# Optimization experiments

Measured on AMD Instinct MI355X. Metric: run time of the kernel, lower is better.

Reference implementation:

```python
import jax, jax.numpy as jnp
import numpy as np

EPS = 1e-4
B, C, H, W = 8, 192, 64, 64
HID, DE, N_CLS, CLS_F, E = 256, 64, 8192, 128, 131072
N_IMG = B * H * W


def geolin(x, w):
    # MP_GeoLinear forward: weight-normalized linear, recomputed each call.
    fan = w.shape[1]
    n = jnp.linalg.norm(w, axis=1, keepdims=True)           # per-output-row norm (fp32)
    wn = w / (EPS + n / np.sqrt(fan))                       # normalize() with alpha=1/sqrt(fan)
    return x @ (wn * (1.0 / np.sqrt(fan))).T                # gain/sqrt(fan_in)


def mp_silu(x):
    return jax.nn.silu(x) / 0.596


def mp_cat(a, b, t=0.5):
    Na, Nb = a.shape[1], b.shape[1]
    Cc = np.sqrt((Na + Nb) / ((1 - t) ** 2 + t ** 2))
    return jnp.concatenate([(Cc / np.sqrt(Na) * (1 - t)) * a,
                            (Cc / np.sqrt(Nb) * t) * b], axis=1)


def hetero_conv(x_src, x_dst, src, dst, ea, wl, wr, n_dst):
    # MP_HIPGnnConv: gather -> mp_cat with edge_attr -> mean aggregate -> lin_l,
    # mp_sum with lin_r(x_dst) -> L2 normalize (normalize=True).
    msg = mp_cat(x_src[src], ea)                            # [E, HID+DE]
    s = jax.ops.segment_sum(msg, dst, num_segments=n_dst)
    cnt = jax.ops.segment_sum(jnp.ones((msg.shape[0],), msg.dtype), dst, num_segments=n_dst)
    agg = s / jnp.maximum(cnt, 1.0)[:, None]                # scatter-mean (empty rows -> 0)
    out = (geolin(agg, wl) + geolin(x_dst, wr)) / np.sqrt(2.0)  # mp_sum(t=0.5)
    return out / jnp.maximum(jnp.linalg.norm(out, axis=-1, keepdims=True), 1e-12)


def forward(x, class_x, ea_c2i, ea_i2c,
            w_in_img, w_in_cls,
            wl_c2i_1, wr_c2i_1, wl_i2c_1, wr_i2c_1,
            wl_c2i_2, wr_c2i_2, wl_i2c_2, wr_i2c_2,
            w_out_img, w_out_cls,
            src_c2i, dst_c2i, src_i2c, dst_i2c):
    b, c, h, w = x.shape
    n_img = b * h * w
    n_cls = class_x.shape[0]
    # image pixels become 'image_node' features: [B,C,H,W] -> [B*H*W, C]
    h_img = geolin(jnp.transpose(x, (0, 2, 3, 1)).reshape(-1, c), w_in_img)
    h_cls = geolin(class_x, w_in_cls)
    layers = [(wl_c2i_1, wr_c2i_1, wl_i2c_1, wr_i2c_1),
              (wl_c2i_2, wr_c2i_2, wl_i2c_2, wr_i2c_2)]
    for wl_ci, wr_ci, wl_ic, wr_ic in layers:
        a_img, a_cls = mp_silu(h_img), mp_silu(h_cls)
        h_img = hetero_conv(a_cls, a_img, src_c2i, dst_c2i, ea_c2i, wl_ci, wr_ci, n_img)
        h_cls = hetero_conv(a_img, a_cls, src_i2c, dst_i2c, ea_i2c, wl_ic, wr_ic, n_cls)
    out_img = geolin(h_img, w_out_img).reshape(b, h, w, -1)
    out_img = jnp.transpose(out_img, (0, 3, 1, 2))          # extract_image_nodes
    out_cls = geolin(h_cls, w_out_cls)
    return out_img, out_cls


def setup_inputs() -> dict:
    key = jax.random.key(0)
    ks = jax.random.split(key, 24)
    d = {
        'x': jax.random.normal(ks[0], (B, C, H, W), jnp.float32),
        'class_x': jax.random.normal(ks[1], (N_CLS, CLS_F), jnp.float32),
        'ea_c2i': jax.random.normal(ks[2], (E, DE), jnp.float32),
        'ea_i2c': jax.random.normal(ks[3], (E, DE), jnp.float32),
        'w_in_img': jax.random.normal(ks[4], (HID, C), jnp.float32),
        'w_in_cls': jax.random.normal(ks[5], (HID, CLS_F), jnp.float32),
        'wl_c2i_1': jax.random.normal(ks[6], (HID, HID + DE), jnp.float32),
        'wr_c2i_1': jax.random.normal(ks[7], (HID, HID), jnp.float32),
        'wl_i2c_1': jax.random.normal(ks[8], (HID, HID + DE), jnp.float32),
        'wr_i2c_1': jax.random.normal(ks[9], (HID, HID), jnp.float32),
        'wl_c2i_2': jax.random.normal(ks[10], (HID, HID + DE), jnp.float32),
        'wr_c2i_2': jax.random.normal(ks[11], (HID, HID), jnp.float32),
        'wl_i2c_2': jax.random.normal(ks[12], (HID, HID + DE), jnp.float32),
        'wr_i2c_2': jax.random.normal(ks[13], (HID, HID), jnp.float32),
        'w_out_img': jax.random.normal(ks[14], (HID, HID), jnp.float32),
        'w_out_cls': jax.random.normal(ks[15], (HID, HID), jnp.float32),
        'src_c2i': jax.random.randint(ks[16], (E,), 0, N_CLS, jnp.int32),
        'dst_c2i': jax.random.randint(ks[17], (E,), 0, N_IMG, jnp.int32),
        'src_i2c': jax.random.randint(ks[18], (E,), 0, N_IMG, jnp.int32),
        'dst_i2c': jax.random.randint(ks[19], (E,), 0, N_CLS, jnp.int32),
    }
    return d


def reference(x, class_x, ea_c2i, ea_i2c,
              w_in_img, w_in_cls,
              wl_c2i_1, wr_c2i_1, wl_i2c_1, wr_i2c_1,
              wl_c2i_2, wr_c2i_2, wl_i2c_2, wr_i2c_2,
              w_out_img, w_out_cls,
              src_c2i, dst_c2i, src_i2c, dst_i2c):
    return forward(x, class_x, ea_c2i, ea_i2c,
                   w_in_img, w_in_cls,
                   wl_c2i_1, wr_c2i_1, wl_i2c_1, wr_i2c_1,
                   wl_c2i_2, wr_c2i_2, wl_i2c_2, wr_i2c_2,
                   w_out_img, w_out_cls,
                   src_c2i, dst_c2i, src_i2c, dst_i2c)
```

## Files before the change

kernel.cpp:

```cpp
#include <hip/hip_runtime.h>
#include <cmath>

constexpr int CIN  = 192;
constexpr int HW   = 4096;
constexpr int NIMG = 32768;
constexpr int NCLS = 8192;
constexpr int NE   = 131072;

#define EPSW 1e-4f
#define ALPHA 0.7905694150420949f
#define BETA  1.5811388300841898f
#define SILU_INV 1.6778523489932886f

using bf16x8 = __attribute__((ext_vector_type(8))) __bf16;
using f32x4  = __attribute__((ext_vector_type(4))) float;

__device__ __forceinline__ ushort f2bf(float f) {
  uint u = __float_as_uint(f);
  u = (u + 0x7FFFu + ((u >> 16) & 1u)) >> 16;
  return (ushort)u;
}
__device__ __forceinline__ float bf2f(ushort h) {
  return __uint_as_float(((uint)h) << 16);
}
__device__ __forceinline__ float wave_red_sum(float v) {
  #pragma unroll
  for (int off = 32; off > 0; off >>= 1) v += __shfl_xor(v, off, 64);
  return v;
}
__device__ __forceinline__ int wave_red_sumi(int v) {
  #pragma unroll
  for (int off = 32; off > 0; off >>= 1) v += __shfl_xor(v, off, 64);
  return v;
}
__device__ __forceinline__ uint4 packbf8(float a0, float a1, float a2, float a3,
                                         float a4, float a5, float a6, float a7) {
  uint4 r;
  r.x = (uint)f2bf(a0) | ((uint)f2bf(a1) << 16);
  r.y = (uint)f2bf(a2) | ((uint)f2bf(a3) << 16);
  r.z = (uint)f2bf(a4) | ((uint)f2bf(a5) << 16);
  r.w = (uint)f2bf(a6) | ((uint)f2bf(a7) << 16);
  return r;
}

struct WNA {
  const float* w[12];
  ushort* o[12];
  int F[12];
  int os[12];
  int oo[12];
};
__global__ __launch_bounds__(256) void pre_k(WNA a,
                                             const int* __restrict__ d1,
                                             const int* __restrict__ d2,
                                             int* __restrict__ c1,
                                             int* __restrict__ c2) {
  const int bx = blockIdx.x, t = threadIdx.x;
  if (bx < 768) {
    const int wi = bx >> 6;
    const int row = ((bx & 63) << 2) + (t >> 6);
    const int lane = t & 63;
    const int F = a.F[wi];
    const float* wr = a.w[wi] + (size_t)row * F;
    float ss = 0.f;
    for (int f = lane; f < F; f += 64) { float v = wr[f]; ss += v * v; }
    ss = wave_red_sum(ss);
    const float scale = 1.0f / (EPSW * sqrtf((float)F) + sqrtf(ss));
    ushort* o = a.o[wi] + (size_t)row * a.os[wi] + a.oo[wi];
    for (int f = lane; f < F; f += 64) o[f] = f2bf(wr[f] * scale);
  } else {
    const int e = (bx - 768) * 256 + t;
    atomicAdd(&c1[d1[e]], 1);
    atomicAdd(&c2[d2[e]], 1);
  }
}

__global__ __launch_bounds__(256) void scanA_k(const int* __restrict__ cnt,
                                               int* __restrict__ st_img,
                                               int* __restrict__ st_cls,
                                               int* __restrict__ bsum) {
  const int bid = blockIdx.x;
  const bool cls = bid >= 32;
  const int* c = cnt + (cls ? NIMG : 0);
  int* s = cls ? st_cls : st_img;
  const int base = (cls ? bid - 32 : bid) * 1024;
  const int t = threadIdx.x, lane = t & 63, wid = t >> 6;
  int4 v = *(const int4*)(c + base + t * 4);
  const int i0 = v.x, i1 = i0 + v.y, i2 = i1 + v.z, i3 = i2 + v.w;
  int x = i3;
  #pragma unroll
  for (int off = 1; off < 64; off <<= 1) {
    int y = __shfl_up(x, off, 64);
    if (lane >= off) x += y;
  }
  const int pre = x - i3;
  __shared__ int wt[4];
  if (lane == 63) wt[wid] = x;
  __syncthreads();
  int woff = 0;
  #pragma unroll
  for (int i = 0; i < 4; ++i) if (i < wid) woff += wt[i];
  const int b = woff + pre;
  int4 o = { b, b + i0, b + i1, b + i2 };
  *(int4*)(s + base + t * 4) = o;
  if (t == 255) bsum[bid] = woff + x;
}

__global__ __launch_bounds__(256) void scanC_k(const int* __restrict__ bsum,
                                               int* __restrict__ st_img,
                                               int* __restrict__ st_cls) {
  const int bid = blockIdx.x;
  const bool cls = bid >= 32;
  const int seg0 = cls ? 32 : 0;
  const int t = threadIdx.x;
  __shared__ int off_s;
  if (t < 64) {
    int v = (t < bid - seg0) ? bsum[seg0 + t] : 0;
    v = wave_red_sumi(v);
    if (t == 0) off_s = v;
  }
  __syncthreads();
  const int off = off_s;
  int* s = cls ? st_cls : st_img;
  const int base = (cls ? bid - 32 : bid) * 1024;
  int4 v = *(int4*)(s + base + t * 4);
  v.x += off; v.y += off; v.z += off; v.w += off;
  *(int4*)(s + base + t * 4) = v;
  if (bid == 0 && t == 0) { st_img[NIMG] = NE; st_cls[NCLS] = NE; }
}

__global__ void fill2_k(const int* __restrict__ dst1, const int* __restrict__ src1,
                        const int* __restrict__ st1, int* __restrict__ cur1,
                        int2* __restrict__ eix1,
                        const int* __restrict__ dst2, const int* __restrict__ src2,
                        const int* __restrict__ st2, int* __restrict__ cur2,
                        int2* __restrict__ eix2) {
  int e = blockIdx.x * 256 + threadIdx.x;
  int d = dst1[e];
  int p = atomicAdd(&cur1[d], 1);
  eix1[st1[d] + p] = make_int2(e, src1[e]);
  d = dst2[e];
  p = atomicAdd(&cur2[d], 1);
  eix2[st2[d] + p] = make_int2(e, src2[e]);
}

__global__ __launch_bounds__(256) void agg2_k(
    const ushort* __restrict__ Aimg, const ushort* __restrict__ Acls,
    const int2* __restrict__ eix_ci, const int2* __restrict__ eix_ic,
    const int* __restrict__ st_img, const int* __restrict__ st_cls,
    ushort* __restrict__ agg_img, ushort* __restrict__ agg_cls,
    const float* __restrict__ ea_ci, const float* __restrict__ ea_ic,
    ushort* __restrict__ eam_img, ushort* __restrict__ eam_cls, int do_eam) {
  const int row  = blockIdx.x * 4 + (threadIdx.x >> 6);
  const int lane = threadIdx.x & 63;
  const ushort* Hs; const int2* eix; const int* st; ushort* out;
  const float* EA; ushort* oute; int r;
  if (row < NIMG) { r = row;        Hs = Acls; eix = eix_ci; st = st_img;
                    out = agg_img + (size_t)r * 256; EA = ea_ci;
                    oute = eam_img + (size_t)r * 64; }
  else            { r = row - NIMG; Hs = Aimg; eix = eix_ic; st = st_cls;
                    out = agg_cls + (size_t)r * 256; EA = ea_ic;
                    oute = eam_cls + (size_t)r * 64; }
  const int s0 = st[r], s1 = st[r + 1];
  float a0 = 0, a1 = 0, a2 = 0, a3 = 0, ae = 0;
  for (int j = s0; j < s1; j += 4) {
    const int i1 = min(j + 1, s1 - 1), i2 = min(j + 2, s1 - 1), i3 = min(j + 3, s1 - 1);
    const int2 e0 = eix[j], e1 = eix[i1], e2 = eix[i2], e3 = eix[i3];
    const float w1 = (j + 1 < s1) ? 1.f : 0.f;
    const float w2 = (j + 2 < s1) ? 1.f : 0.f;
    const float w3 = (j + 3 < s1) ? 1.f : 0.f;
    ushort4 h0 = *(const ushort4*)(Hs + (size_t)e0.y * 256 + lane * 4);
    ushort4 h1 = *(const ushort4*)(Hs + (size_t)e1.y * 256 + lane * 4);
    ushort4 h2 = *(const ushort4*)(Hs + (size_t)e2.y * 256 + lane * 4);
    ushort4 h3 = *(const ushort4*)(Hs + (size_t)e3.y * 256 + lane * 4);
    a0 += bf2f(h0.x) + w1 * bf2f(h1.x) + w2 * bf2f(h2.x) + w3 * bf2f(h3.x);
    a1 += bf2f(h0.y) + w1 * bf2f(h1.y) + w2 * bf2f(h2.y) + w3 * bf2f(h3.y);
    a2 += bf2f(h0.z) + w1 * bf2f(h1.z) + w2 * bf2f(h2.z) + w3 * bf2f(h3.z);
    a3 += bf2f(h0.w) + w1 * bf2f(h1.w) + w2 * bf2f(h2.w) + w3 * bf2f(h3.w);
    if (do_eam) {
      ae += EA[(size_t)e0.x * 64 + lane] + w1 * EA[(size_t)e1.x * 64 + lane]
          + w2 * EA[(size_t)e2.x * 64 + lane] + w3 * EA[(size_t)e3.x * 64 + lane];
    }
  }
  const float inv = 1.0f / fmaxf((float)(s1 - s0), 1.0f);
  const float c = ALPHA * inv;
  ushort4 o = { f2bf(a0 * c), f2bf(a1 * c), f2bf(a2 * c), f2bf(a3 * c) };
  *(ushort4*)(out + lane * 4) = o;
  if (do_eam) oute[lane] = f2bf(ae * BETA * inv);
}

__device__ __forceinline__ int lds_swz(int row, int kbyte) {
  return ((row << 6) + kbyte) ^ ((row & 7) << 4);
}

struct FJ {
  const ushort* AD; const ushort* AG; const ushort* EAM;
  const float* AF; const ushort* B; ushort* O;
  int K, a_mode, do_norm, do_silu;
};

__device__ __forceinline__ void fgemm_body(const FJ J, int bx, char* ldsb) {
  ushort* As = (ushort*)ldsb;
  ushort* Bs = (ushort*)(ldsb + 8192);
  const int t    = threadIdx.x;
  const int row0 = bx * 128;
  const int srowA = t >> 2, skA = (t & 3) * 8;
  const int srowB = t >> 1, skB = (t & 1) * 16;
  const int wid = t >> 6, lane = t & 63;
  const int wr = (wid >> 2) * 64, wcq = wid & 3, wc = wcq * 64;
  const int l15 = lane & 15, q = lane >> 4, lk16 = q * 16;
  const int K = J.K;
  f32x4 acc[4][4] = {};

  uint4 areg, breg0, breg1;
  auto loadA = [&](int k0) {
    const int row = row0 + srowA;
    if (J.a_mode == 2) {
      const int kk = k0 + skA;
      const ushort* p = (kk < 256) ? J.AG + (size_t)row * 256 + kk
                      : (kk < 320) ? J.EAM + (size_t)row * 64 + (kk - 256)
                                   : J.AD + (size_t)row * 256 + (kk - 320);
      areg = *(const uint4*)p;
    } else if (J.a_mode == 3) {
      const float* p = J.AF + (size_t)row * K + k0 + skA;
      float4 f0 = *(const float4*)p;
      float4 f1 = *(const float4*)(p + 4);
      areg = packbf8(f0.x, f0.y, f0.z, f0.w, f1.x, f1.y, f1.z, f1.w);
    } else {
      const int b = row >> 12, hw = row & 4095;
      const float* p = J.AF + ((size_t)(b * CIN + k0 + skA)) * HW + hw;
      float f0 = p[0], f1 = p[HW], f2 = p[2 * HW], f3 = p[3 * HW];
      float f4 = p[4 * HW], f5 = p[5 * HW], f6 = p[6 * HW], f7 = p[7 * HW];
      areg = packbf8(f0, f1, f2, f3, f4, f5, f6, f7);
    }
  };
  auto loadB = [&](int k0) {
    const ushort* p = J.B + (size_t)srowB * K + k0 + skB;
    breg0 = *(const uint4*)p;
    breg1 = *(const uint4*)(p + 8);
  };

  loadA(0); loadB(0);
  for (int k0 = 0; k0 < K; k0 += 32) {
    __syncthreads();
    *(uint4*)(ldsb + lds_swz(srowA, skA * 2)) = areg;
    *(uint4*)((char*)Bs + lds_swz(srowB, skB * 2)) = breg0;
    *(uint4*)((char*)Bs + lds_swz(srowB, skB * 2 + 16)) = breg1;
    __syncthreads();
    if (k0 + 32 < K) { loadA(k0 + 32); loadB(k0 + 32); }
    bf16x8 af[4], bfr[4];
    #pragma unroll
    for (int m = 0; m < 4; ++m)
      af[m] = *(const bf16x8*)((const char*)As + lds_swz(wr + m * 16 + l15, lk16));
    #pragma unroll
    for (int n = 0; n < 4; ++n)
      bfr[n] = *(const bf16x8*)((const char*)Bs + lds_swz(wc + n * 16 + l15, lk16));
    #pragma unroll
    for (int m = 0; m < 4; ++m)
      #pragma unroll
      for (int n = 0; n < 4; ++n)
        acc[m][n] = __builtin_amdgcn_mfma_f32_16x16x32_bf16(af[m], bfr[n], acc[m][n], 0, 0, 0);
  }

  float sc_row[4][4];
  #pragma unroll
  for (int m = 0; m < 4; ++m)
    #pragma unroll
    for (int j = 0; j < 4; ++j) sc_row[m][j] = 1.0f;
  if (J.do_norm) {
    __syncthreads();
    float* part = (float*)ldsb;
    #pragma unroll
    for (int m = 0; m < 4; ++m)
      #pragma unroll
      for (int j = 0; j < 4; ++j) {
        float ss = 0.f;
        #pragma unroll
        for (int n = 0; n < 4; ++n) { float v = acc[m][n][j]; ss += v * v; }
        ss += __shfl_xor(ss, 1, 64); ss += __shfl_xor(ss, 2, 64);
        ss += __shfl_xor(ss, 4, 64); ss += __shfl_xor(ss, 8, 64);
        if (l15 == 0) part[(wr + m * 16 + q * 4 + j) * 4 + wcq] = ss;
      }
    __syncthreads();
    #pragma unroll
    for (int m = 0; m < 4; ++m)
      #pragma unroll
      for (int j = 0; j < 4; ++j) {
        float4 p4 = *(float4*)&part[(wr + m * 16 + q * 4 + j) * 4];
        sc_row[m][j] = 1.0f / fmaxf(sqrtf(p4.x + p4.y + p4.z + p4.w), 1e-12f);
      }
  }
  #pragma unroll
  for (int m = 0; m < 4; ++m)
    #pragma unroll
    for (int j = 0; j < 4; ++j) {
      const int r = row0 + wr + m * 16 + q * 4 + j;
      #pragma unroll
      for (int n = 0; n < 4; ++n) {
        float v = acc[m][n][j] * sc_row[m][j];
        if (J.do_silu) v = (v / (1.0f + __expf(-v))) * SILU_INV;
        J.O[(size_t)r * 256 + wc + n * 16 + l15] = f2bf(v);
      }
    }
}

__global__ __launch_bounds__(512) void fgemm2_k(FJ j0, FJ j1, int n0) {
  __shared__ char ldsb[24576];
  const int bx = blockIdx.x;
  if (bx < n0) fgemm_body(j0, bx, ldsb);
  else         fgemm_body(j1, bx - n0, ldsb);
}

__device__ __forceinline__ void mgemm_body(
    const ushort* __restrict__ A, const ushort* __restrict__ B,
    float* __restrict__ C, int K, int ldc, int c_mode,
    int row0, int col0, char* ldsb) {
  ushort* As = (ushort*)ldsb;
  ushort* Bs = (ushort*)(ldsb + 8192);
  const int t    = threadIdx.x;
  const int srow = t >> 1;
  const int skh  = (t & 1) * 16;
  const int w    = t >> 6, lane = t & 63;
  const int wr   = (w >> 1) * 64, wc = (w & 1) * 64;
  const int l15  = lane & 15, lk16 = (lane >> 4) * 16;
  f32x4 acc[4][4] = {};

  uint4 ar0, ar1, br0, br1;
  auto loadA = [&](int k0) {
    const ushort* p = A + (size_t)(row0 + srow) * K + k0 + skh;
    ar0 = *(const uint4*)(p);
    ar1 = *(const uint4*)(p + 8);
  };
  auto loadB = [&](int k0) {
    const ushort* p = B + (size_t)(col0 + srow) * K + k0 + skh;
    br0 = *(const uint4*)(p);
    br1 = *(const uint4*)(p + 8);
  };

  loadA(0); loadB(0);
  for (int k0 = 0; k0 < K; k0 += 32) {
    __syncthreads();
    *(uint4*)((char*)As + lds_swz(srow, skh * 2))      = ar0;
    *(uint4*)((char*)As + lds_swz(srow, skh * 2 + 16)) = ar1;
    *(uint4*)((char*)Bs + lds_swz(srow, skh * 2))      = br0;
    *(uint4*)((char*)Bs + lds_swz(srow, skh * 2 + 16)) = br1;
    __syncthreads();
    if (k0 + 32 < K) { loadA(k0 + 32); loadB(k0 + 32); }
    bf16x8 af[4], bfr[4];
    #pragma unroll
    for (int m = 0; m < 4; ++m)
      af[m] = *(const bf16x8*)((const char*)As + lds_swz(wr + m * 16 + l15, lk16));
    #pragma unroll
    for (int n = 0; n < 4; ++n)
      bfr[n] = *(const bf16x8*)((const char*)Bs + lds_swz(wc + n * 16 + l15, lk16));
    #pragma unroll
    for (int m = 0; m < 4; ++m)
      #pragma unroll
      for (int n = 0; n < 4; ++n)
        acc[m][n] = __builtin_amdgcn_mfma_f32_16x16x32_bf16(af[m], bfr[n], acc[m][n], 0, 0, 0);
  }

  #pragma unroll
  for (int m = 0; m < 4; ++m) {
    const int rbase = row0 + wr + m * 16 + (lane >> 4) * 4;
    #pragma unroll
    for (int n = 0; n < 4; ++n) {
      const int col = col0 + wc + n * 16 + l15;
      #pragma unroll
      for (int j = 0; j < 4; ++j) {
        const int r = rbase + j;
        if (c_mode == 1)
          C[((size_t)(col >> 12) * 256 + r) * 4096 + (col & 4095)] = acc[m][n][j];
        else
          C[(size_t)r * ldc + col] = acc[m][n][j];
      }
    }
  }
}

__global__ __launch_bounds__(256) void outproj_k(
    const ushort* __restrict__ Wimg, const ushort* __restrict__ Himg,
    float* __restrict__ Oimg, const ushort* __restrict__ Hcls,
    const ushort* __restrict__ Wcls, float* __restrict__ Ocls) {
  __shared__ char ldsb[16384];
  const int bx = blockIdx.x;
  if (bx < 512)
    mgemm_body(Wimg, Himg, Oimg, 256, 0, 1, (bx & 1) * 128, (bx >> 1) * 128, ldsb);
  else {
    const int b2 = bx - 512;
    mgemm_body(Hcls, Wcls, Ocls, 256, 256, 2, (b2 >> 1) * 128, (b2 & 1) * 128, ldsb);
  }
}

extern "C" void kernel_launch(void* const* d_in, const int* in_sizes, int n_in,
                              void* d_out, int out_size, void* d_ws, size_t ws_size,
                              hipStream_t stream) {
  const float* x        = (const float*)d_in[0];
  const float* class_x  = (const float*)d_in[1];
  const float* ea_c2i   = (const float*)d_in[2];
  const float* ea_i2c   = (const float*)d_in[3];
  const int* src_c2i = (const int*)d_in[16];
  const int* dst_c2i = (const int*)d_in[17];
  const int* src_i2c = (const int*)d_in[18];
  const int* dst_i2c = (const int*)d_in[19];

  float* ws = (float*)d_ws;
  size_t off = 0;
  auto alloc = [&](size_t n) { float* p = ws + off; off += (n + 15) & ~(size_t)15; return p; };

  ushort* A_img   = (ushort*)alloc((size_t)NIMG * 128);
  ushort* A_cls   = (ushort*)alloc((size_t)NCLS * 128);
  ushort* H_img   = (ushort*)alloc((size_t)NIMG * 128);
  ushort* H_cls   = (ushort*)alloc((size_t)NCLS * 128);
  ushort* agg_img = (ushort*)alloc((size_t)NIMG * 128);
  ushort* agg_cls = (ushort*)alloc((size_t)NCLS * 128);
  ushort* eam_img = (ushort*)alloc((size_t)NIMG * 32);
  ushort* eam_cls = (ushort*)alloc((size_t)NCLS * 32);
  int* cnt       = (int*)alloc(2 * (NIMG + NCLS));
  int* cur       = cnt + (NIMG + NCLS);
  int* bsum      = (int*)alloc(48);
  int* st_img    = (int*)alloc(NIMG + 1 + NCLS + 1 + 14);
  int* st_cls    = st_img + NIMG + 1;
  int2* eix_c2i  = (int2*)alloc((size_t)NE * 2);
  int2* eix_i2c  = (int2*)alloc((size_t)NE * 2);
  ushort* wn_in_img  = (ushort*)alloc(256 * 96);
  ushort* wn_in_cls  = (ushort*)alloc(256 * 64);
  ushort* wcat0      = (ushort*)alloc(256 * 288);
  ushort* wcat1      = (ushort*)alloc(256 * 288);
  ushort* wcat2      = (ushort*)alloc(256 * 288);
  ushort* wcat3      = (ushort*)alloc(256 * 288);
  ushort* wn_out_img = (ushort*)alloc(256 * 128);
  ushort* wn_out_cls = (ushort*)alloc(256 * 128);

  const dim3 blk(256);

  hipMemsetAsync(cnt, 0, (size_t)2 * (NIMG + NCLS) * sizeof(int), stream);
  WNA wa;
  const float* wsrc[12] = { (const float*)d_in[4], (const float*)d_in[5],
                            (const float*)d_in[6], (const float*)d_in[7],
                            (const float*)d_in[8], (const float*)d_in[9],
                            (const float*)d_in[10], (const float*)d_in[11],
                            (const float*)d_in[12], (const float*)d_in[13],
                            (const float*)d_in[14], (const float*)d_in[15] };
  ushort* wdst[12] = { wn_in_img, wn_in_cls, wcat0, wcat0, wcat1, wcat1,
                       wcat2, wcat2, wcat3, wcat3, wn_out_img, wn_out_cls };
  const int wF[12]  = { 192, 128, 320, 256, 320, 256, 320, 256, 320, 256, 256, 256 };
  const int wOS[12] = { 192, 128, 576, 576, 576, 576, 576, 576, 576, 576, 256, 256 };
  const int wOO[12] = { 0, 0, 0, 320, 0, 320, 0, 320, 0, 320, 0, 0 };
  for (int i = 0; i < 12; ++i) {
    wa.w[i] = wsrc[i]; wa.o[i] = wdst[i]; wa.F[i] = wF[i]; wa.os[i] = wOS[i]; wa.oo[i] = wOO[i];
  }
  pre_k<<<768 + NE / 256, blk, 0, stream>>>(wa, dst_c2i, dst_i2c, cnt, cnt + NIMG);

  scanA_k<<<40, blk, 0, stream>>>(cnt, st_img, st_cls, bsum);
  scanC_k<<<40, blk, 0, stream>>>(bsum, st_img, st_cls);
  fill2_k<<<NE / 256, blk, 0, stream>>>(dst_c2i, src_c2i, st_img, cur, eix_c2i,
                                        dst_i2c, src_i2c, st_cls, cur + NIMG, eix_i2c);

  FJ jin0 = { nullptr, nullptr, nullptr, x,       wn_in_img, A_img, 192, 1, 0, 1 };
  FJ jin1 = { nullptr, nullptr, nullptr, class_x, wn_in_cls, A_cls, 128, 3, 0, 1 };
  fgemm2_k<<<NIMG / 128 + NCLS / 128, 512, 0, stream>>>(jin0, jin1, NIMG / 128);

  agg2_k<<<(NIMG + NCLS) / 4, blk, 0, stream>>>(A_img, A_cls, eix_c2i, eix_i2c,
                                                st_img, st_cls, agg_img, agg_cls,
                                                ea_c2i, ea_i2c, eam_img, eam_cls, 1);
  FJ jc10 = { A_img, agg_img, eam_img, nullptr, wcat0, A_img, 576, 2, 1, 1 };
  FJ jc11 = { A_cls, agg_cls, eam_cls, nullptr, wcat1, A_cls, 576, 2, 1, 1 };
  fgemm2_k<<<NIMG / 128 + NCLS / 128, 512, 0, stream>>>(jc10, jc11, NIMG / 128);

  agg2_k<<<(NIMG + NCLS) / 4, blk, 0, stream>>>(A_img, A_cls, eix_c2i, eix_i2c,
                                                st_img, st_cls, agg_img, agg_cls,
                                                nullptr, nullptr, nullptr, nullptr, 0);
  FJ jc20 = { A_img, agg_img, eam_img, nullptr, wcat2, H_img, 576, 2, 1, 0 };
  FJ jc21 = { A_cls, agg_cls, eam_cls, nullptr, wcat3, H_cls, 576, 2, 1, 0 };
  fgemm2_k<<<NIMG / 128 + NCLS / 128, 512, 0, stream>>>(jc20, jc21, NIMG / 128);

  float* out_img = (float*)d_out;
  float* out_cls = (float*)d_out + (size_t)NIMG * 256;
  outproj_k<<<640, blk, 0, stream>>>(wn_out_img, H_img, out_img,
                                     H_cls, wn_out_cls, out_cls);
}
```

Before: 227.0 us.

## Unify GEMMs into double-buffered 64x256 tile kernel with pre-converted bf16 inputs

Replaces the 128x256 fused GEMM (512 threads) and the separate output-projection GEMM with one 256-thread kernel. It uses 64x256 tiles and double-buffers the LDS tiles, so each k-step needs one barrier instead of two. The input image is transposed and converted to bf16 in the preprocessing kernel, and class_x is converted there too, so GEMM A-loads become contiguous vector loads instead of strided fp32 gathers. This adds extra global write and read traffic for the staged inputs. Each block now covers fewer rows, which changes B-tile reuse and occupancy.

```diff
diff --git a/kernel.cpp b/kernel.cpp
--- a/kernel.cpp
+++ b/kernel.cpp
@@ -32,15 +32,6 @@
   #pragma unroll
   for (int off = 32; off > 0; off >>= 1) v += __shfl_xor(v, off, 64);
   return v;
-}
-__device__ __forceinline__ uint4 packbf8(float a0, float a1, float a2, float a3,
-                                         float a4, float a5, float a6, float a7) {
-  uint4 r;
-  r.x = (uint)f2bf(a0) | ((uint)f2bf(a1) << 16);
-  r.y = (uint)f2bf(a2) | ((uint)f2bf(a3) << 16);
-  r.z = (uint)f2bf(a4) | ((uint)f2bf(a5) << 16);
-  r.w = (uint)f2bf(a6) | ((uint)f2bf(a7) << 16);
-  return r;
 }
 
 struct WNA {
@@ -54,7 +45,12 @@
                                              const int* __restrict__ d1,
                                              const int* __restrict__ d2,
                                              int* __restrict__ c1,
-                                             int* __restrict__ c2) {
+                                             int* __restrict__ c2,
+                                             const float* __restrict__ x,
+                                             ushort* __restrict__ Xin,
+                                             const float* __restrict__ clsx,
+                                             ushort* __restrict__ clsb) {
+  __shared__ ushort T[192 * 65];
   const int bx = blockIdx.x, t = threadIdx.x;
   if (bx < 768) {
     const int wi = bx >> 6;
@@ -68,10 +64,31 @@
     const float scale = 1.0f / (EPSW * sqrtf((float)F) + sqrtf(ss));
     ushort* o = a.o[wi] + (size_t)row * a.os[wi] + a.oo[wi];
     for (int f = lane; f < F; f += 64) o[f] = f2bf(wr[f] * scale);
-  } else {
+  } else if (bx < 1280) {
     const int e = (bx - 768) * 256 + t;
     atomicAdd(&c1[d1[e]], 1);
     atomicAdd(&c2[d2[e]], 1);
+  } else if (bx < 1792) {
+    const int b2 = bx - 1280;
+    const int b = b2 >> 6, hw0 = (b2 & 63) * 64;
+    const float* xb = x + (size_t)b * CIN * HW;
+    for (int idx = t; idx < CIN * 64; idx += 256) {
+      int c = idx >> 6, p = idx & 63;
+      T[c * 65 + p] = f2bf(xb[(size_t)c * HW + hw0 + p]);
+    }
+    __syncthreads();
+    ushort* ob = Xin + ((size_t)b * HW + hw0) * CIN;
+    for (int idx = t; idx < CIN * 64; idx += 256) {
+      int p = idx / CIN, c = idx - p * CIN;
+      ob[(size_t)p * CIN + c] = T[c * 65 + p];
+    }
+  } else {
+    const int b3 = bx - 1792;
+    for (int i4 = b3 * 256 + t; i4 < (NCLS * 128) / 4; i4 += 128 * 256) {
+      float4 v = *(const float4*)(clsx + (size_t)i4 * 4);
+      ushort4 o = { f2bf(v.x), f2bf(v.y), f2bf(v.z), f2bf(v.w) };
+      *(ushort4*)(clsb + (size_t)i4 * 4) = o;
+    }
   }
 }
 
@@ -193,73 +210,73 @@
   return ((row << 6) + kbyte) ^ ((row & 7) << 4);
 }
 
-struct FJ {
-  const ushort* AD; const ushort* AG; const ushort* EAM;
-  const float* AF; const ushort* B; ushort* O;
-  int K, a_mode, do_norm, do_silu;
+struct GJ {
+  const ushort* A; const ushort* AG; const ushort* EAM; const ushort* B;
+  void* O;
+  int K, a_mode, c_mode, do_norm, do_silu, nrt;
 };
 
-__device__ __forceinline__ void fgemm_body(const FJ J, int bx, char* ldsb) {
-  ushort* As = (ushort*)ldsb;
-  ushort* Bs = (ushort*)(ldsb + 8192);
-  const int t    = threadIdx.x;
-  const int row0 = bx * 128;
-  const int srowA = t >> 2, skA = (t & 3) * 8;
-  const int srowB = t >> 1, skB = (t & 1) * 16;
+__device__ __forceinline__ void gemm_body(const GJ J, int bx, char* ldsb) {
+  const int t = threadIdx.x;
+  const int row0 = (bx % J.nrt) * 64;
+  const int col0 = (bx / J.nrt) * 256;
+  const int srowA = t >> 2, skA16 = (t & 3) * 16;
   const int wid = t >> 6, lane = t & 63;
-  const int wr = (wid >> 2) * 64, wcq = wid & 3, wc = wcq * 64;
+  const int wc = wid * 64;
   const int l15 = lane & 15, q = lane >> 4, lk16 = q * 16;
   const int K = J.K;
   f32x4 acc[4][4] = {};
-
-  uint4 areg, breg0, breg1;
+  uint4 ar, br0, br1, br2, br3;
+
   auto loadA = [&](int k0) {
     const int row = row0 + srowA;
+    const int kk = k0 + (skA16 >> 1);
     if (J.a_mode == 2) {
-      const int kk = k0 + skA;
       const ushort* p = (kk < 256) ? J.AG + (size_t)row * 256 + kk
                       : (kk < 320) ? J.EAM + (size_t)row * 64 + (kk - 256)
-                                   : J.AD + (size_t)row * 256 + (kk - 320);
-      areg = *(const uint4*)p;
-    } else if (J.a_mode == 3) {
-      const float* p = J.AF + (size_t)row * K + k0 + skA;
-      float4 f0 = *(const float4*)p;
-      float4 f1 = *(const float4*)(p + 4);
-      areg = packbf8(f0.x, f0.y, f0.z, f0.w, f1.x, f1.y, f1.z, f1.w);
+                                   : J.A + (size_t)row * 256 + (kk - 320);
+      ar = *(const uint4*)p;
     } else {
-      const int b = row >> 12, hw = row & 4095;
-      const float* p = J.AF + ((size_t)(b * CIN + k0 + skA)) * HW + hw;
-      float f0 = p[0], f1 = p[HW], f2 = p[2 * HW], f3 = p[3 * HW];
-      float f4 = p[4 * HW], f5 = p[5 * HW], f6 = p[6 * HW], f7 = p[7 * HW];
-      areg = packbf8(f0, f1, f2, f3, f4, f5, f6, f7);
+      ar = *(const uint4*)(J.A + (size_t)row * K + kk);
     }
   };
   auto loadB = [&](int k0) {
-    const ushort* p = J.B + (size_t)srowB * K + k0 + skB;
-    breg0 = *(const uint4*)p;
-    breg1 = *(const uint4*)(p + 8);
+    const ushort* p = J.B + (size_t)(col0 + t) * K + k0;
+    br0 = *(const uint4*)p;       br1 = *(const uint4*)(p + 8);
+    br2 = *(const uint4*)(p + 16); br3 = *(const uint4*)(p + 24);
   };
+  auto stage = [&](int buf) {
+    *(uint4*)(ldsb + buf * 4096 + lds_swz(srowA, skA16)) = ar;
+    char* bs = ldsb + 8192 + buf * 16384;
+    *(uint4*)(bs + lds_swz(t, 0))  = br0;
+    *(uint4*)(bs + lds_swz(t, 16)) = br1;
+    *(uint4*)(bs + lds_swz(t, 32)) = br2;
+    *(uint4*)(bs + lds_swz(t, 48)) = br3;
+  };
 
   loadA(0); loadB(0);
+  stage(0);
+  int cur = 0;
   for (int k0 = 0; k0 < K; k0 += 32) {
     __syncthreads();
-    *(uint4*)(ldsb + lds_swz(srowA, skA * 2)) = areg;
-    *(uint4*)((char*)Bs + lds_swz(srowB, skB * 2)) = breg0;
-    *(uint4*)((char*)Bs + lds_swz(srowB, skB * 2 + 16)) = breg1;
-    __syncthreads();
-    if (k0 + 32 < K) { loadA(k0 + 32); loadB(k0 + 32); }
+    const bool more = (k0 + 32) < K;
+    if (more) { loadA(k0 + 32); loadB(k0 + 32); }
+    const char* as = ldsb + cur * 4096;
+    const char* bs = ldsb + 8192 + cur * 16384;
     bf16x8 af[4], bfr[4];
     #pragma unroll
     for (int m = 0; m < 4; ++m)
-      af[m] = *(const bf16x8*)((const char*)As + lds_swz(wr + m * 16 + l15, lk16));
+      af[m] = *(const bf16x8*)(as + lds_swz(m * 16 + l15, lk16));
     #pragma unroll
     for (int n = 0; n < 4; ++n)
-      bfr[n] = *(const bf16x8*)((const char*)Bs + lds_swz(wc + n * 16 + l15, lk16));
+      bfr[n] = *(const bf16x8*)(bs + lds_swz(wc + n * 16 + l15, lk16));
     #pragma unroll
     for (int m = 0; m < 4; ++m)
       #pragma unroll
       for (int n = 0; n < 4; ++n)
         acc[m][n] = __builtin_amdgcn_mfma_f32_16x16x32_bf16(af[m], bfr[n], acc[m][n], 0, 0, 0);
+    if (more) stage(cur ^ 1);
+    cur ^= 1;
   }
 
   float sc_row[4][4];
@@ -279,117 +296,45 @@
         for (int n = 0; n < 4; ++n) { float v = acc[m][n][j]; ss += v * v; }
         ss += __shfl_xor(ss, 1, 64); ss += __shfl_xor(ss, 2, 64);
         ss += __shfl_xor(ss, 4, 64); ss += __shfl_xor(ss, 8, 64);
-        if (l15 == 0) part[(wr + m * 16 + q * 4 + j) * 4 + wcq] = ss;
+        if (l15 == 0) part[(m * 16 + q * 4 + j) * 4 + wid] = ss;
       }
     __syncthreads();
     #pragma unroll
     for (int m = 0; m < 4; ++m)
       #pragma unroll
       for (int j = 0; j < 4; ++j) {
-        float4 p4 = *(float4*)&part[(wr + m * 16 + q * 4 + j) * 4];
+        float4 p4 = *(float4*)&part[(m * 16 + q * 4 + j) * 4];
         sc_row[m][j] = 1.0f / fmaxf(sqrtf(p4.x + p4.y + p4.z + p4.w), 1e-12f);
       }
   }
+  ushort* Ob = (ushort*)J.O;
+  float*  Of = (float*)J.O;
   #pragma unroll
   for (int m = 0; m < 4; ++m)
     #pragma unroll
     for (int j = 0; j < 4; ++j) {
-      const int r = row0 + wr + m * 16 + q * 4 + j;
+      const int r = row0 + m * 16 + q * 4 + j;
       #pragma unroll
       for (int n = 0; n < 4; ++n) {
+        const int col = col0 + wc + n * 16 + l15;
         float v = acc[m][n][j] * sc_row[m][j];
-        if (J.do_silu) v = (v / (1.0f + __expf(-v))) * SILU_INV;
-        J.O[(size_t)r * 256 + wc + n * 16 + l15] = f2bf(v);
+        if (J.c_mode == 0) {
+          if (J.do_silu) v = (v / (1.0f + __expf(-v))) * SILU_INV;
+          Ob[(size_t)r * 256 + col] = f2bf(v);
+        } else if (J.c_mode == 1) {
+          Of[((size_t)(col >> 12) * 256 + r) * 4096 + (col & 4095)] = v;
+        } else {
+          Of[(size_t)r * 256 + col] = v;
+        }
       }
     }
 }
 
-__global__ __launch_bounds__(512) void fgemm2_k(FJ j0, FJ j1, int n0) {
-  __shared__ char ldsb[24576];
+__global__ __launch_bounds__(256) void gemm2_k(GJ j0, GJ j1, int n0) {
+  __shared__ char ldsb[40960];
   const int bx = blockIdx.x;
-  if (bx < n0) fgemm_body(j0, bx, ldsb);
-  else         fgemm_body(j1, bx - n0, ldsb);
-}
-
-__device__ __forceinline__ void mgemm_body(
-    const ushort* __restrict__ A, const ushort* __restrict__ B,
-    float* __restrict__ C, int K, int ldc, int c_mode,
-    int row0, int col0, char* ldsb) {
-  ushort* As = (ushort*)ldsb;
-  ushort* Bs = (ushort*)(ldsb + 8192);
-  const int t    = threadIdx.x;
-  const int srow = t >> 1;
-  const int skh  = (t & 1) * 16;
-  const int w    = t >> 6, lane = t & 63;
-  const int wr   = (w >> 1) * 64, wc = (w & 1) * 64;
-  const int l15  = lane & 15, lk16 = (lane >> 4) * 16;
-  f32x4 acc[4][4] = {};
-
-  uint4 ar0, ar1, br0, br1;
-  auto loadA = [&](int k0) {
-    const ushort* p = A + (size_t)(row0 + srow) * K + k0 + skh;
-    ar0 = *(const uint4*)(p);
-    ar1 = *(const uint4*)(p + 8);
-  };
-  auto loadB = [&](int k0) {
-    const ushort* p = B + (size_t)(col0 + srow) * K + k0 + skh;
-    br0 = *(const uint4*)(p);
-    br1 = *(const uint4*)(p + 8);
-  };
-
-  loadA(0); loadB(0);
-  for (int k0 = 0; k0 < K; k0 += 32) {
-    __syncthreads();
-    *(uint4*)((char*)As + lds_swz(srow, skh * 2))      = ar0;
-    *(uint4*)((char*)As + lds_swz(srow, skh * 2 + 16)) = ar1;
-    *(uint4*)((char*)Bs + lds_swz(srow, skh * 2))      = br0;
-    *(uint4*)((char*)Bs + lds_swz(srow, skh * 2 + 16)) = br1;
-    __syncthreads();
-    if (k0 + 32 < K) { loadA(k0 + 32); loadB(k0 + 32); }
-    bf16x8 af[4], bfr[4];
-    #pragma unroll
-    for (int m = 0; m < 4; ++m)
-      af[m] = *(const bf16x8*)((const char*)As + lds_swz(wr + m * 16 + l15, lk16));
-    #pragma unroll
-    for (int n = 0; n < 4; ++n)
-      bfr[n] = *(const bf16x8*)((const char*)Bs + lds_swz(wc + n * 16 + l15, lk16));
-    #pragma unroll
-    for (int m = 0; m < 4; ++m)
-      #pragma unroll
-      for (int n = 0; n < 4; ++n)
-        acc[m][n] = __builtin_amdgcn_mfma_f32_16x16x32_bf16(af[m], bfr[n], acc[m][n], 0, 0, 0);
-  }
-
-  #pragma unroll
-  for (int m = 0; m < 4; ++m) {
-    const int rbase = row0 + wr + m * 16 + (lane >> 4) * 4;
-    #pragma unroll
-    for (int n = 0; n < 4; ++n) {
-      const int col = col0 + wc + n * 16 + l15;
-      #pragma unroll
-      for (int j = 0; j < 4; ++j) {
-        const int r = rbase + j;
-        if (c_mode == 1)
-          C[((size_t)(col >> 12) * 256 + r) * 4096 + (col & 4095)] = acc[m][n][j];
-        else
-          C[(size_t)r * ldc + col] = acc[m][n][j];
-      }
-    }
-  }
-}
-
-__global__ __launch_bounds__(256) void outproj_k(
-    const ushort* __restrict__ Wimg, const ushort* __restrict__ Himg,
-    float* __restrict__ Oimg, const ushort* __restrict__ Hcls,
-    const ushort* __restrict__ Wcls, float* __restrict__ Ocls) {
-  __shared__ char ldsb[16384];
-  const int bx = blockIdx.x;
-  if (bx < 512)
-    mgemm_body(Wimg, Himg, Oimg, 256, 0, 1, (bx & 1) * 128, (bx >> 1) * 128, ldsb);
-  else {
-    const int b2 = bx - 512;
-    mgemm_body(Hcls, Wcls, Ocls, 256, 256, 2, (b2 >> 1) * 128, (b2 & 1) * 128, ldsb);
-  }
+  if (bx < n0) gemm_body(j0, bx, ldsb);
+  else         gemm_body(j1, bx - n0, ldsb);
 }
 
 extern "C" void kernel_launch(void* const* d_in, const int* in_sizes, int n_in,
@@ -431,6 +376,8 @@
   ushort* wcat3      = (ushort*)alloc(256 * 288);
   ushort* wn_out_img = (ushort*)alloc(256 * 128);
   ushort* wn_out_cls = (ushort*)alloc(256 * 128);
+  ushort* Xin      = agg_img;
+  ushort* class_bf = agg_cls;
 
   const dim3 blk(256);
 
@@ -450,33 +397,35 @@
   for (int i = 0; i < 12; ++i) {
     wa.w[i] = wsrc[i]; wa.o[i] = wdst[i]; wa.F[i] = wF[i]; wa.os[i] = wOS[i]; wa.oo[i] = wOO[i];
   }
-  pre_k<<<768 + NE / 256, blk, 0, stream>>>(wa, dst_c2i, dst_i2c, cnt, cnt + NIMG);
+  pre_k<<<1920, blk, 0, stream>>>(wa, dst_c2i, dst_i2c, cnt, cnt + NIMG,
+                                  x, Xin, class_x, class_bf);
 
   scanA_k<<<40, blk, 0, stream>>>(cnt, st_img, st_cls, bsum);
   scanC_k<<<40, blk, 0, stream>>>(bsum, st_img, st_cls);
   fill2_k<<<NE / 256, blk, 0, stream>>>(dst_c2i, src_c2i, st_img, cur, eix_c2i,
                                         dst_i2c, src_i2c, st_cls, cur + NIMG, eix_i2c);
 
-  FJ jin0 = { nullptr, nullptr, nullptr, x,       wn_in_img, A_img, 192, 1, 0, 1 };
-  FJ jin1 = { nullptr, nullptr, nullptr, class_x, wn_in_cls, A_cls, 128, 3, 0, 1 };
-  fgemm2_k<<<NIMG / 128 + NCLS / 128, 512, 0, stream>>>(jin0, jin1, NIMG / 128);
+  GJ jin0 = { Xin,      nullptr, nullptr, wn_in_img, A_img, 192, 0, 0, 0, 1, 512 };
+  GJ jin1 = { class_bf, nullptr, nullptr, wn_in_cls, A_cls, 128, 0, 0, 0, 1, 128 };
+  gemm2_k<<<640, blk, 0, stream>>>(jin0, jin1, 512);
 
   agg2_k<<<(NIMG + NCLS) / 4, blk, 0, stream>>>(A_img, A_cls, eix_c2i, eix_i2c,
                                                 st_img, st_cls, agg_img, agg_cls,
                                                 ea_c2i, ea_i2c, eam_img, eam_cls, 1);
-  FJ jc10 = { A_img, agg_img, eam_img, nullptr, wcat0, A_img, 576, 2, 1, 1 };
-  FJ jc11 = { A_cls, agg_cls, eam_cls, nullptr, wcat1, A_cls, 576, 2, 1, 1 };
-  fgemm2_k<<<NIMG / 128 + NCLS / 128, 512, 0, stream>>>(jc10, jc11, NIMG / 128);
+  GJ jc10 = { A_img, agg_img, eam_img, wcat0, A_img, 576, 2, 0, 1, 1, 512 };
+  GJ jc11 = { A_cls, agg_cls, eam_cls, wcat1, A_cls, 576, 2, 0, 1, 1, 128 };
+  gemm2_k<<<640, blk, 0, stream>>>(jc10, jc11, 512);
 
   agg2_k<<<(NIMG + NCLS) / 4, blk, 0, stream>>>(A_img, A_cls, eix_c2i, eix_i2c,
                                                 st_img, st_cls, agg_img, agg_cls,
                                                 nullptr, nullptr, nullptr, nullptr, 0);
-  FJ jc20 = { A_img, agg_img, eam_img, nullptr, wcat2, H_img, 576, 2, 1, 0 };
-  FJ jc21 = { A_cls, agg_cls, eam_cls, nullptr, wcat3, H_cls, 576, 2, 1, 0 };
-  fgemm2_k<<<NIMG / 128 + NCLS / 128, 512, 0, stream>>>(jc20, jc21, NIMG / 128);
+  GJ jc20 = { A_img, agg_img, eam_img, wcat2, H_img, 576, 2, 0, 1, 0, 512 };
+  GJ jc21 = { A_cls, agg_cls, eam_cls, wcat3, H_cls, 576, 2, 0, 1, 0, 128 };
+  gemm2_k<<<640, blk, 0, stream>>>(jc20, jc21, 512);
 
   float* out_img = (float*)d_out;
   float* out_cls = (float*)d_out + (size_t)NIMG * 256;
-  outproj_k<<<640, blk, 0, stream>>>(wn_out_img, H_img, out_img,
-                                     H_cls, wn_out_cls, out_cls);
-}
+  GJ jo0 = { wn_out_img, nullptr, nullptr, H_img,      out_img, 256, 0, 1, 0, 0, 4 };
+  GJ jo1 = { H_cls,      nullptr, nullptr, wn_out_cls, out_cls, 256, 0, 2, 0, 0, 128 };
+  gemm2_k<<<640, blk, 0, stream>>>(jo0, jo1, 512);
+}
```

Result: slower. 284.4 us (+25.3%).
